# Kernel tuning notes

Hardware: AMD Instinct MI355X
Metric: run time of the kernel (lower is better)

Reference implementation:

```python
import jax, jax.numpy as jnp
from jax import lax
import numpy as np

EMBED_DIM = 512
KERNEL_SIZE = 8
B, S = 16, 4096


def setup_inputs() -> dict:
    key = jax.random.key(0)
    k1, k2, k3, k4, k5 = jax.random.split(key, 5)
    bound = 1.0 / np.sqrt(EMBED_DIM)
    x = jax.random.normal(k1, (B, S, EMBED_DIM), dtype=jnp.float32)
    W_ih = jax.random.uniform(k2, (EMBED_DIM, EMBED_DIM), jnp.float32, -bound, bound)
    W_hh = jax.random.uniform(k3, (EMBED_DIM, EMBED_DIM), jnp.float32, -bound, bound)
    b_ih = jax.random.uniform(k4, (EMBED_DIM,), jnp.float32, -bound, bound)
    b_hh = jax.random.uniform(k5, (EMBED_DIM,), jnp.float32, -bound, bound)
    return {"x": x, "W_ih": W_ih, "W_hh": W_hh, "b_ih": b_ih, "b_hh": b_hh}


def reference(x, W_ih, W_hh, b_ih, b_hh):
    # RNNPool.forward(x, mask=False): split seq into windows of KERNEL_SIZE,
    # run a vanilla tanh RNN (zero initial state) on each window, keep last h.
    Bd, Sd, E = x.shape
    stride = KERNEL_SIZE
    nw = Sd // stride
    # All windows are independent -> batch them: [B*nw, stride, E]
    xw = x.reshape(Bd * nw, stride, E)
    # Precompute input projection + both biases once: [B*nw, stride, E]
    pre = jnp.einsum("nte,he->nth", xw, W_ih) + (b_ih + b_hh)

    def step(h, p_t):
        h = jnp.tanh(p_t + h @ W_hh.T)
        return h, None

    h0 = jnp.zeros((Bd * nw, E), dtype=x.dtype)
    hT, _ = lax.scan(step, h0, jnp.swapaxes(pre, 0, 1))  # scan over stride steps
    return hT.reshape(Bd, nw, E)
```

## Files before the change

kernel.cpp:

```cpp
#include <hip/hip_runtime.h>
#include <hip/hip_bf16.h>
#include <stdint.h>


#define E_DIM 512
#define KSIZE 8
#define R_WIN 32
#define NBLK  256

typedef __attribute__((ext_vector_type(8))) _Float16       f16x8;
typedef __attribute__((ext_vector_type(4))) float          f32x4;
typedef __attribute__((ext_vector_type(4))) float          fv4;
typedef __attribute__((ext_vector_type(4))) unsigned short u16x4;
typedef __attribute__((ext_vector_type(8))) unsigned short u16x8;

typedef __attribute__((address_space(1))) const uint32_t glb_u32;
typedef __attribute__((address_space(3))) uint32_t       lds_u32;

__device__ __forceinline__ unsigned short f2h(float f) {
  return __builtin_bit_cast(unsigned short, (_Float16)f);
}
__device__ __forceinline__ float h2f(unsigned short u) {
  return (float)__builtin_bit_cast(_Float16, u);
}
__device__ __forceinline__ float tanh_fast(float v) {
  return 1.0f - 2.0f / (1.0f + __expf(2.0f * v));
}
__device__ __forceinline__ int swz(int row) { return (row ^ (row >> 1)) & 7; }

__global__ void pack_kernel(const float* __restrict__ Wih, const float* __restrict__ Whh,
                            const float* __restrict__ bih, const float* __restrict__ bhh,
                            unsigned short* __restrict__ wpack, float* __restrict__ bias) {
  int tid = blockIdx.x * 256 + threadIdx.x;
  int l = tid & 63;
  int s = (tid >> 6) & 15;
  int n = (tid >> 10) & 31;
  int m = tid >> 15;
  const float* W = m ? Whh : Wih;
  int row = n * 16 + (l & 15);
  int k0  = s * 32 + (l >> 4) * 8;
  const float* src = W + row * E_DIM + k0;
  u16x8 u;
  #pragma unroll
  for (int j = 0; j < 8; ++j) u[j] = f2h(src[j]);
  size_t dst = (((size_t)m * 16 + s) * 32 + n) * 512 + (size_t)l * 8;
  *reinterpret_cast<u16x8*>(wpack + dst) = u;
  if (tid < E_DIM) bias[tid] = bih[tid] + bhh[tid];
}

#define PRE_FRAG(bt, mt, nt) ((((size_t)(bt) * 2 + (mt)) * 32 + (nt)) * 256)

__global__ __launch_bounds__(512, 4)
void pre_kernel(const float* __restrict__ x,
                const unsigned short* __restrict__ wpack,
                const float* __restrict__ bias,
                unsigned short* __restrict__ prep) {
  __shared__ unsigned short x_lds[R_WIN * E_DIM];

  const int bt   = blockIdx.x;
  const int b    = bt >> 3;
  const int t    = bt & 7;
  const int w0   = b * R_WIN;
  const int tid  = threadIdx.x;
  const int lane = tid & 63;
  const int wid  = tid >> 6;
  const int l15  = lane & 15;
  const int a5   = lane >> 4;
  const int nt0  = wid * 4;

  float bias_r[4];
  #pragma unroll
  for (int n = 0; n < 4; ++n) bias_r[n] = bias[(nt0 + n) * 16 + l15];

  {
    const int srow = tid >> 4;
    const int sc4  = tid & 15;
    const fv4* src4 = reinterpret_cast<const fv4*>(
        x + (size_t)((w0 + srow) * KSIZE + t) * E_DIM);
    #pragma unroll
    for (int j = 0; j < 8; ++j) {
      fv4 v = __builtin_nontemporal_load(&src4[sc4 + 16 * j]);
      int col  = (sc4 + 16 * j) * 4;
      int idx  = srow * E_DIM + (((col >> 3) ^ swz(srow)) << 3) + (col & 7);
      u16x4 u;
      u[0] = f2h(v.x); u[1] = f2h(v.y); u[2] = f2h(v.z); u[3] = f2h(v.w);
      *reinterpret_cast<u16x4*>(&x_lds[idx]) = u;
    }
  }
  __syncthreads();

  f32x4 acc[2][4];
  #pragma unroll
  for (int mt = 0; mt < 2; ++mt)
    #pragma unroll
    for (int n = 0; n < 4; ++n) acc[mt][n] = (f32x4){0.f, 0.f, 0.f, 0.f};

  #pragma unroll
  for (int s = 0; s < 16; ++s) {
    int u0 = s * 4 + a5;
    int ia = l15 * E_DIM + ((u0 ^ swz(l15)) << 3);
    f16x8 A0 = *reinterpret_cast<const f16x8*>(&x_lds[ia]);
    f16x8 A1 = *reinterpret_cast<const f16x8*>(&x_lds[ia + 16 * E_DIM]);
    const unsigned short* wsl = wpack + ((size_t)s * 32 + nt0) * 512 + lane * 8;
    #pragma unroll
    for (int n = 0; n < 4; ++n) {
      f16x8 Bf = *reinterpret_cast<const f16x8*>(wsl + n * 512);
      acc[0][n] = __builtin_amdgcn_mfma_f32_16x16x32_f16(A0, Bf, acc[0][n], 0, 0, 0);
      acc[1][n] = __builtin_amdgcn_mfma_f32_16x16x32_f16(A1, Bf, acc[1][n], 0, 0, 0);
    }
  }

  #pragma unroll
  for (int mt = 0; mt < 2; ++mt)
    #pragma unroll
    for (int n = 0; n < 4; ++n) {
      u16x4 v;
      #pragma unroll
      for (int r = 0; r < 4; ++r) v[r] = f2h(acc[mt][n][r] + bias_r[n]);
      __builtin_nontemporal_store(v,
          reinterpret_cast<u16x4*>(&prep[PRE_FRAG(bt, mt, nt0 + n) + lane * 4]));
    }
}

__global__ __launch_bounds__(1024, 4)
void rec_kernel(const unsigned short* __restrict__ prep,
                const unsigned short* __restrict__ wpack,
                float* __restrict__ out) {
  __shared__ unsigned short h_buf[R_WIN * E_DIM];
  __shared__ unsigned short w_lds[3][16 * 1024];

  const int b    = blockIdx.x;
  const int w0   = b * R_WIN;
  const int tid  = threadIdx.x;
  const int lane = tid & 63;
  const int wid  = tid >> 6;
  const int l15  = lane & 15;
  const int a5   = lane >> 4;
  const int nt0  = wid * 2;

  const char* wbase = (const char*)(wpack + ((size_t)16 * 32) * 512);
  #define STAGE(s)                                                                  \
    do {                                                                            \
      const char* _src = wbase + (((size_t)(s) * 32 + nt0) * 1024) + lane * 16;     \
      unsigned short* _dst = &w_lds[(s) % 3][wid * 1024];                           \
      __builtin_amdgcn_global_load_lds((glb_u32*)_src, (lds_u32*)_dst, 16, 0, 0);   \
      __builtin_amdgcn_global_load_lds((glb_u32*)(_src + 1024),                     \
                                       (lds_u32*)(_dst + 512), 16, 0, 0);           \
    } while (0)

  #pragma unroll
  for (int mt = 0; mt < 2; ++mt)
    #pragma unroll
    for (int n = 0; n < 2; ++n) {
      u16x4 p = __builtin_nontemporal_load(reinterpret_cast<const u16x4*>(
          &prep[PRE_FRAG(b * 8 + 0, mt, nt0 + n) + lane * 4]));
      int ncol = (nt0 + n) * 16 + l15;
      int ub = ncol >> 3, co = ncol & 7;
      #pragma unroll
      for (int r = 0; r < 4; ++r) {
        int row = mt * 16 + a5 * 4 + r;
        int idx = row * E_DIM + ((ub ^ swz(row)) << 3) + co;
        h_buf[idx] = f2h(tanh_fast(h2f(p[r])));
      }
    }

  u16x4 nxt[2][2];
  #pragma unroll
  for (int mt = 0; mt < 2; ++mt)
    #pragma unroll
    for (int n = 0; n < 2; ++n)
      nxt[mt][n] = __builtin_nontemporal_load(reinterpret_cast<const u16x4*>(
          &prep[PRE_FRAG(b * 8 + 1, mt, nt0 + n) + lane * 4]));

  __syncthreads();

  for (int t = 1; t < KSIZE; ++t) {
    f32x4 acc[2][2];
    #pragma unroll
    for (int mt = 0; mt < 2; ++mt)
      #pragma unroll
      for (int n = 0; n < 2; ++n) {
        #pragma unroll
        for (int r = 0; r < 4; ++r) acc[mt][n][r] = h2f(nxt[mt][n][r]);
      }

    STAGE(0);
    STAGE(1);
    STAGE(2);
    asm volatile("s_waitcnt vmcnt(4)" ::: "memory");
    f16x8 Wa0, Wa1, Ha0, Ha1;
    f16x8 Wb0, Wb1, Hb0, Hb1;
    {
      const unsigned short* wsl = &w_lds[0][wid * 1024 + lane * 8];
      Wa0 = *reinterpret_cast<const f16x8*>(wsl);
      Wa1 = *reinterpret_cast<const f16x8*>(wsl + 512);
      int ia0 = l15 * E_DIM + ((a5 ^ swz(l15)) << 3);
      int ia1 = (16 + l15) * E_DIM + ((a5 ^ swz(16 + l15)) << 3);
      Ha0 = *reinterpret_cast<const f16x8*>(&h_buf[ia0]);
      Ha1 = *reinterpret_cast<const f16x8*>(&h_buf[ia1]);
    }

    #pragma unroll
    for (int s = 0; s < 16; ++s) {
      asm volatile("s_waitcnt lgkmcnt(0)" ::: "memory");
      if (s + 3 < 16) STAGE(s + 3);
      if (s < 13)       asm volatile("s_waitcnt vmcnt(4)" ::: "memory");
      else if (s == 13) asm volatile("s_waitcnt vmcnt(2)" ::: "memory");
      else if (s == 14) asm volatile("s_waitcnt vmcnt(0)" ::: "memory");
      if (s < 15) {
        const unsigned short* wsl = &w_lds[(s + 1) % 3][wid * 1024 + lane * 8];
        Wb0 = *reinterpret_cast<const f16x8*>(wsl);
        Wb1 = *reinterpret_cast<const f16x8*>(wsl + 512);
        int u0  = (s + 1) * 4 + a5;
        int ia0 = l15 * E_DIM + ((u0 ^ swz(l15)) << 3);
        int ia1 = (16 + l15) * E_DIM + ((u0 ^ swz(16 + l15)) << 3);
        Hb0 = *reinterpret_cast<const f16x8*>(&h_buf[ia0]);
        Hb1 = *reinterpret_cast<const f16x8*>(&h_buf[ia1]);
      }
      acc[0][0] = __builtin_amdgcn_mfma_f32_16x16x32_f16(Ha0, Wa0, acc[0][0], 0, 0, 0);
      acc[0][1] = __builtin_amdgcn_mfma_f32_16x16x32_f16(Ha0, Wa1, acc[0][1], 0, 0, 0);
      acc[1][0] = __builtin_amdgcn_mfma_f32_16x16x32_f16(Ha1, Wa0, acc[1][0], 0, 0, 0);
      acc[1][1] = __builtin_amdgcn_mfma_f32_16x16x32_f16(Ha1, Wa1, acc[1][1], 0, 0, 0);
      Wa0 = Wb0; Wa1 = Wb1; Ha0 = Hb0; Ha1 = Hb1;
    }

    if (t == KSIZE - 1) {
      #pragma unroll
      for (int mt = 0; mt < 2; ++mt)
        #pragma unroll
        for (int n = 0; n < 2; ++n) {
          int ncol = (nt0 + n) * 16 + l15;
          #pragma unroll
          for (int r = 0; r < 4; ++r) {
            int row = mt * 16 + a5 * 4 + r;
            out[(size_t)(w0 + row) * E_DIM + ncol] = tanh_fast(acc[mt][n][r]);
          }
        }
    } else {
      __syncthreads();

      #pragma unroll
      for (int mt = 0; mt < 2; ++mt)
        #pragma unroll
        for (int n = 0; n < 2; ++n)
          nxt[mt][n] = __builtin_nontemporal_load(reinterpret_cast<const u16x4*>(
              &prep[PRE_FRAG(b * 8 + t + 1, mt, nt0 + n) + lane * 4]));

      #pragma unroll
      for (int mt = 0; mt < 2; ++mt)
        #pragma unroll
        for (int n = 0; n < 2; ++n) {
          int ncol = (nt0 + n) * 16 + l15;
          int ub = ncol >> 3, co = ncol & 7;
          #pragma unroll
          for (int r = 0; r < 4; ++r) {
            int row = mt * 16 + a5 * 4 + r;
            int idx = row * E_DIM + ((ub ^ swz(row)) << 3) + co;
            h_buf[idx] = f2h(tanh_fast(acc[mt][n][r]));
          }
        }
      __syncthreads();
    }
  }
  #undef STAGE
}

__global__ __launch_bounds__(512, 1)
void rnnpool_fused(const float* __restrict__ x,
                   const unsigned short* __restrict__ wpack,
                   const float* __restrict__ bias,
                   float* __restrict__ out) {
  __shared__ unsigned short x_lds[R_WIN * E_DIM];
  __shared__ unsigned short h_lds[R_WIN * E_DIM];

  const int tid  = threadIdx.x;
  const int lane = tid & 63;
  const int wid  = tid >> 6;
  const int w0   = blockIdx.x * R_WIN;
  const int l15 = lane & 15;
  const int a5  = lane >> 4;
  const int nt0 = wid * 4;

  float bias_r[4];
  #pragma unroll
  for (int n = 0; n < 4; ++n) bias_r[n] = bias[(nt0 + n) * 16 + l15];

  const int srow = tid >> 4;
  const int sc4  = tid & 15;

  for (int t = 0; t < KSIZE; ++t) {
    {
      const fv4* src4 = reinterpret_cast<const fv4*>(
          x + (size_t)((w0 + srow) * KSIZE + t) * E_DIM);
      #pragma unroll
      for (int j = 0; j < 8; ++j) {
        fv4 v = src4[sc4 + 16 * j];
        int col  = (sc4 + 16 * j) * 4;
        int idx  = srow * E_DIM + (((col >> 3) ^ swz(srow)) << 3) + (col & 7);
        u16x4 u;
        u[0] = f2h(v.x); u[1] = f2h(v.y); u[2] = f2h(v.z); u[3] = f2h(v.w);
        *reinterpret_cast<u16x4*>(&x_lds[idx]) = u;
      }
    }
    __syncthreads();

    f32x4 acc[2][4];
    #pragma unroll
    for (int mt = 0; mt < 2; ++mt)
      #pragma unroll
      for (int n = 0; n < 4; ++n) acc[mt][n] = (f32x4){0.f, 0.f, 0.f, 0.f};

    #pragma unroll
    for (int s = 0; s < 16; ++s) {
      int u0 = s * 4 + a5;
      int ia = l15 * E_DIM + ((u0 ^ swz(l15)) << 3);
      f16x8 A0 = *reinterpret_cast<const f16x8*>(&x_lds[ia]);
      f16x8 A1 = *reinterpret_cast<const f16x8*>(&x_lds[ia + 16 * E_DIM]);
      const unsigned short* wsl = wpack + ((size_t)s * 32 + nt0) * 512 + lane * 8;
      #pragma unroll
      for (int n = 0; n < 4; ++n) {
        f16x8 Bf = *reinterpret_cast<const f16x8*>(wsl + n * 512);
        acc[0][n] = __builtin_amdgcn_mfma_f32_16x16x32_f16(A0, Bf, acc[0][n], 0, 0, 0);
        acc[1][n] = __builtin_amdgcn_mfma_f32_16x16x32_f16(A1, Bf, acc[1][n], 0, 0, 0);
      }
    }

    if (t > 0) {
      #pragma unroll
      for (int s = 0; s < 16; ++s) {
        int u0 = s * 4 + a5;
        int ia = l15 * E_DIM + ((u0 ^ swz(l15)) << 3);
        f16x8 H0 = *reinterpret_cast<const f16x8*>(&h_lds[ia]);
        f16x8 H1 = *reinterpret_cast<const f16x8*>(&h_lds[ia + 16 * E_DIM]);
        const unsigned short* wsl = wpack + ((size_t)(16 + s) * 32 + nt0) * 512 + lane * 8;
        #pragma unroll
        for (int n = 0; n < 4; ++n) {
          f16x8 Bf = *reinterpret_cast<const f16x8*>(wsl + n * 512);
          acc[0][n] = __builtin_amdgcn_mfma_f32_16x16x32_f16(H0, Bf, acc[0][n], 0, 0, 0);
          acc[1][n] = __builtin_amdgcn_mfma_f32_16x16x32_f16(H1, Bf, acc[1][n], 0, 0, 0);
        }
      }
    }
    __syncthreads();

    if (t == KSIZE - 1) {
      #pragma unroll
      for (int mt = 0; mt < 2; ++mt)
        #pragma unroll
        for (int n = 0; n < 4; ++n) {
          int ncol = (nt0 + n) * 16 + l15;
          #pragma unroll
          for (int r = 0; r < 4; ++r) {
            int row = mt * 16 + a5 * 4 + r;
            out[(size_t)(w0 + row) * E_DIM + ncol] = tanh_fast(acc[mt][n][r] + bias_r[n]);
          }
        }
    } else {
      #pragma unroll
      for (int mt = 0; mt < 2; ++mt)
        #pragma unroll
        for (int n = 0; n < 4; ++n) {
          int ncol = (nt0 + n) * 16 + l15;
          int ub = ncol >> 3, co = ncol & 7;
          #pragma unroll
          for (int r = 0; r < 4; ++r) {
            int row = mt * 16 + a5 * 4 + r;
            int idx = row * E_DIM + ((ub ^ swz(row)) << 3) + co;
            h_lds[idx] = f2h(tanh_fast(acc[mt][n][r] + bias_r[n]));
          }
        }
      __syncthreads();
    }
  }
}

extern "C" void kernel_launch(void* const* d_in, const int* in_sizes, int n_in,
                              void* d_out, int out_size, void* d_ws, size_t ws_size,
                              hipStream_t stream) {
  const float* x   = (const float*)d_in[0];
  const float* Wih = (const float*)d_in[1];
  const float* Whh = (const float*)d_in[2];
  const float* bih = (const float*)d_in[3];
  const float* bhh = (const float*)d_in[4];
  float* out = (float*)d_out;

  const size_t PRE_BYTES  = (size_t)33554432 * 2;
  const size_t WPK_BYTES  = (size_t)524288 * 2;
  const size_t NEED       = PRE_BYTES + WPK_BYTES + 4096;

  if (ws_size >= NEED) {
    unsigned short* prep  = (unsigned short*)d_ws;
    unsigned short* wpack = (unsigned short*)((char*)d_ws + PRE_BYTES);
    float*          bias  = (float*)((char*)d_ws + PRE_BYTES + WPK_BYTES);
    pack_kernel<<<256, 256, 0, stream>>>(Wih, Whh, bih, bhh, wpack, bias);
    pre_kernel<<<2048, 512, 0, stream>>>(x, wpack, bias, prep);
    rec_kernel<<<NBLK, 1024, 0, stream>>>(prep, wpack, out);
  } else {
    unsigned short* wpack = (unsigned short*)d_ws;
    float*          bias  = (float*)((char*)d_ws + WPK_BYTES);
    pack_kernel<<<256, 256, 0, stream>>>(Wih, Whh, bih, bhh, wpack, bias);
    rnnpool_fused<<<NBLK, 512, 0, stream>>>(x, wpack, bias, out);
  }
}
```

Before: 171.0 us.

## Halve rec_kernel threads, widen per-wave N tiles, double-buffer hidden state

The recurrence kernel now launches 512 threads per block instead of 1024, and each wave computes four N tiles instead of two. This doubles reuse of each H fragment loaded from LDS across MFMAs. The hidden-state buffer is double-buffered, which removes one __syncthreads per timestep. The weight staging ring shrinks from three slots to two with larger stages, so prefetch depth drops and the per-thread register footprint grows.

Result: faster. 153.7 us (-10.1%).

```diff
diff --git a/kernel.cpp b/kernel.cpp
--- a/kernel.cpp
+++ b/kernel.cpp
@@ -122,12 +122,12 @@
     }
 }
 
-__global__ __launch_bounds__(1024, 4)
+__global__ __launch_bounds__(512, 2)
 void rec_kernel(const unsigned short* __restrict__ prep,
                 const unsigned short* __restrict__ wpack,
                 float* __restrict__ out) {
-  __shared__ unsigned short h_buf[R_WIN * E_DIM];
-  __shared__ unsigned short w_lds[3][16 * 1024];
+  __shared__ unsigned short h_buf[2][R_WIN * E_DIM];
+  __shared__ unsigned short w_ring[2][8 * 2048];
 
   const int b    = blockIdx.x;
   const int w0   = b * R_WIN;
@@ -136,22 +136,26 @@
   const int wid  = tid >> 6;
   const int l15  = lane & 15;
   const int a5   = lane >> 4;
-  const int nt0  = wid * 2;
+  const int nt0  = wid * 4;
 
   const char* wbase = (const char*)(wpack + ((size_t)16 * 32) * 512);
-  #define STAGE(s)                                                                  \
+  #define STAGE(s, p)                                                               \
     do {                                                                            \
       const char* _src = wbase + (((size_t)(s) * 32 + nt0) * 1024) + lane * 16;     \
-      unsigned short* _dst = &w_lds[(s) % 3][wid * 1024];                           \
+      unsigned short* _dst = &w_ring[p][wid * 2048];                                \
       __builtin_amdgcn_global_load_lds((glb_u32*)_src, (lds_u32*)_dst, 16, 0, 0);   \
       __builtin_amdgcn_global_load_lds((glb_u32*)(_src + 1024),                     \
                                        (lds_u32*)(_dst + 512), 16, 0, 0);           \
+      __builtin_amdgcn_global_load_lds((glb_u32*)(_src + 2048),                     \
+                                       (lds_u32*)(_dst + 1024), 16, 0, 0);          \
+      __builtin_amdgcn_global_load_lds((glb_u32*)(_src + 3072),                     \
+                                       (lds_u32*)(_dst + 1536), 16, 0, 0);          \
     } while (0)
 
   #pragma unroll
   for (int mt = 0; mt < 2; ++mt)
     #pragma unroll
-    for (int n = 0; n < 2; ++n) {
+    for (int n = 0; n < 4; ++n) {
       u16x4 p = __builtin_nontemporal_load(reinterpret_cast<const u16x4*>(
           &prep[PRE_FRAG(b * 8 + 0, mt, nt0 + n) + lane * 4]));
       int ncol = (nt0 + n) * 16 + l15;
@@ -160,75 +164,83 @@
       for (int r = 0; r < 4; ++r) {
         int row = mt * 16 + a5 * 4 + r;
         int idx = row * E_DIM + ((ub ^ swz(row)) << 3) + co;
-        h_buf[idx] = f2h(tanh_fast(h2f(p[r])));
-      }
-    }
-
-  u16x4 nxt[2][2];
+        h_buf[0][idx] = f2h(tanh_fast(h2f(p[r])));
+      }
+    }
+
+  u16x4 nxt[2][4];
   #pragma unroll
   for (int mt = 0; mt < 2; ++mt)
     #pragma unroll
-    for (int n = 0; n < 2; ++n)
+    for (int n = 0; n < 4; ++n)
       nxt[mt][n] = __builtin_nontemporal_load(reinterpret_cast<const u16x4*>(
           &prep[PRE_FRAG(b * 8 + 1, mt, nt0 + n) + lane * 4]));
 
   __syncthreads();
 
+  int cur = 0;
   for (int t = 1; t < KSIZE; ++t) {
-    f32x4 acc[2][2];
+    f32x4 acc[2][4];
     #pragma unroll
     for (int mt = 0; mt < 2; ++mt)
       #pragma unroll
-      for (int n = 0; n < 2; ++n) {
+      for (int n = 0; n < 4; ++n) {
         #pragma unroll
         for (int r = 0; r < 4; ++r) acc[mt][n][r] = h2f(nxt[mt][n][r]);
       }
 
-    STAGE(0);
-    STAGE(1);
-    STAGE(2);
+    STAGE(0, 0);
+    STAGE(1, 1);
     asm volatile("s_waitcnt vmcnt(4)" ::: "memory");
-    f16x8 Wa0, Wa1, Ha0, Ha1;
-    f16x8 Wb0, Wb1, Hb0, Hb1;
+    f16x8 Wa0, Wa1, Wa2, Wa3, Ha0, Ha1;
+    f16x8 Wb0, Wb1, Wb2, Wb3, Hb0, Hb1;
     {
-      const unsigned short* wsl = &w_lds[0][wid * 1024 + lane * 8];
+      const unsigned short* wsl = &w_ring[0][wid * 2048 + lane * 8];
       Wa0 = *reinterpret_cast<const f16x8*>(wsl);
       Wa1 = *reinterpret_cast<const f16x8*>(wsl + 512);
+      Wa2 = *reinterpret_cast<const f16x8*>(wsl + 1024);
+      Wa3 = *reinterpret_cast<const f16x8*>(wsl + 1536);
       int ia0 = l15 * E_DIM + ((a5 ^ swz(l15)) << 3);
       int ia1 = (16 + l15) * E_DIM + ((a5 ^ swz(16 + l15)) << 3);
-      Ha0 = *reinterpret_cast<const f16x8*>(&h_buf[ia0]);
-      Ha1 = *reinterpret_cast<const f16x8*>(&h_buf[ia1]);
+      Ha0 = *reinterpret_cast<const f16x8*>(&h_buf[cur][ia0]);
+      Ha1 = *reinterpret_cast<const f16x8*>(&h_buf[cur][ia1]);
     }
 
     #pragma unroll
     for (int s = 0; s < 16; ++s) {
       asm volatile("s_waitcnt lgkmcnt(0)" ::: "memory");
-      if (s + 3 < 16) STAGE(s + 3);
-      if (s < 13)       asm volatile("s_waitcnt vmcnt(4)" ::: "memory");
-      else if (s == 13) asm volatile("s_waitcnt vmcnt(2)" ::: "memory");
+      if (s + 2 < 16) STAGE(s + 2, (s + 2) & 1);
+      if (s < 14)       asm volatile("s_waitcnt vmcnt(4)" ::: "memory");
       else if (s == 14) asm volatile("s_waitcnt vmcnt(0)" ::: "memory");
       if (s < 15) {
-        const unsigned short* wsl = &w_lds[(s + 1) % 3][wid * 1024 + lane * 8];
+        const unsigned short* wsl = &w_ring[(s + 1) & 1][wid * 2048 + lane * 8];
         Wb0 = *reinterpret_cast<const f16x8*>(wsl);
         Wb1 = *reinterpret_cast<const f16x8*>(wsl + 512);
+        Wb2 = *reinterpret_cast<const f16x8*>(wsl + 1024);
+        Wb3 = *reinterpret_cast<const f16x8*>(wsl + 1536);
         int u0  = (s + 1) * 4 + a5;
         int ia0 = l15 * E_DIM + ((u0 ^ swz(l15)) << 3);
         int ia1 = (16 + l15) * E_DIM + ((u0 ^ swz(16 + l15)) << 3);
-        Hb0 = *reinterpret_cast<const f16x8*>(&h_buf[ia0]);
-        Hb1 = *reinterpret_cast<const f16x8*>(&h_buf[ia1]);
+        Hb0 = *reinterpret_cast<const f16x8*>(&h_buf[cur][ia0]);
+        Hb1 = *reinterpret_cast<const f16x8*>(&h_buf[cur][ia1]);
       }
       acc[0][0] = __builtin_amdgcn_mfma_f32_16x16x32_f16(Ha0, Wa0, acc[0][0], 0, 0, 0);
+      acc[1][0] = __builtin_amdgcn_mfma_f32_16x16x32_f16(Ha1, Wa0, acc[1][0], 0, 0, 0);
       acc[0][1] = __builtin_amdgcn_mfma_f32_16x16x32_f16(Ha0, Wa1, acc[0][1], 0, 0, 0);
-      acc[1][0] = __builtin_amdgcn_mfma_f32_16x16x32_f16(Ha1, Wa0, acc[1][0], 0, 0, 0);
       acc[1][1] = __builtin_amdgcn_mfma_f32_16x16x32_f16(Ha1, Wa1, acc[1][1], 0, 0, 0);
-      Wa0 = Wb0; Wa1 = Wb1; Ha0 = Hb0; Ha1 = Hb1;
+      acc[0][2] = __builtin_amdgcn_mfma_f32_16x16x32_f16(Ha0, Wa2, acc[0][2], 0, 0, 0);
+      acc[1][2] = __builtin_amdgcn_mfma_f32_16x16x32_f16(Ha1, Wa2, acc[1][2], 0, 0, 0);
+      acc[0][3] = __builtin_amdgcn_mfma_f32_16x16x32_f16(Ha0, Wa3, acc[0][3], 0, 0, 0);
+      acc[1][3] = __builtin_amdgcn_mfma_f32_16x16x32_f16(Ha1, Wa3, acc[1][3], 0, 0, 0);
+      Wa0 = Wb0; Wa1 = Wb1; Wa2 = Wb2; Wa3 = Wb3;
+      Ha0 = Hb0; Ha1 = Hb1;
     }
 
     if (t == KSIZE - 1) {
       #pragma unroll
       for (int mt = 0; mt < 2; ++mt)
         #pragma unroll
-        for (int n = 0; n < 2; ++n) {
+        for (int n = 0; n < 4; ++n) {
           int ncol = (nt0 + n) * 16 + l15;
           #pragma unroll
           for (int r = 0; r < 4; ++r) {
@@ -237,29 +249,29 @@
           }
         }
     } else {
-      __syncthreads();
-
       #pragma unroll
       for (int mt = 0; mt < 2; ++mt)
         #pragma unroll
-        for (int n = 0; n < 2; ++n)
+        for (int n = 0; n < 4; ++n)
           nxt[mt][n] = __builtin_nontemporal_load(reinterpret_cast<const u16x4*>(
               &prep[PRE_FRAG(b * 8 + t + 1, mt, nt0 + n) + lane * 4]));
 
+      int nb = cur ^ 1;
       #pragma unroll
       for (int mt = 0; mt < 2; ++mt)
         #pragma unroll
-        for (int n = 0; n < 2; ++n) {
+        for (int n = 0; n < 4; ++n) {
           int ncol = (nt0 + n) * 16 + l15;
           int ub = ncol >> 3, co = ncol & 7;
           #pragma unroll
           for (int r = 0; r < 4; ++r) {
             int row = mt * 16 + a5 * 4 + r;
             int idx = row * E_DIM + ((ub ^ swz(row)) << 3) + co;
-            h_buf[idx] = f2h(tanh_fast(acc[mt][n][r]));
+            h_buf[nb][idx] = f2h(tanh_fast(acc[mt][n][r]));
           }
         }
       __syncthreads();
+      cur = nb;
     }
   }
   #undef STAGE
@@ -394,7 +406,7 @@
     float*          bias  = (float*)((char*)d_ws + PRE_BYTES + WPK_BYTES);
     pack_kernel<<<256, 256, 0, stream>>>(Wih, Whh, bih, bhh, wpack, bias);
     pre_kernel<<<2048, 512, 0, stream>>>(x, wpack, bias, prep);
-    rec_kernel<<<NBLK, 1024, 0, stream>>>(prep, wpack, out);
+    rec_kernel<<<NBLK, 512, 0, stream>>>(prep, wpack, out);
   } else {
     unsigned short* wpack = (unsigned short*)d_ws;
     float*          bias  = (float*)((char*)d_ws + WPK_BYTES);
```
